# Performance work log

Measured on AMD Instinct MI355X. Metric: run time of the kernel, lower is better.

## Reference

```python
import jax, jax.numpy as jnp
import numpy as np

# dims
T, N, F, B = 8, 100000, 128, 4096        # snapshots, graph nodes, in_features, seed batch
S1, S2 = 5, 2                             # sampling fanouts (sizes=[5,2])
H1, H2, O, C = 512, 64, 32, 2             # hids=[512,64], out_features, nchannels
TIME_MOD = 2
W_POS, W_NOPOS = 0.6, 0.4
V_TH = 1.0                                # invth=1


@jax.custom_vjp
def spike(v):
    # IF/LIF firing with threshold V_TH (spikingjelly-style heaviside)
    return (v >= V_TH).astype(v.dtype)

def _spike_fwd(v):
    return spike(v), v

def _spike_bwd(v, g):
    # triangle surrogate gradient, alpha=1.0
    return (g * jnp.maximum(0.0, 1.0 - jnp.abs(v - V_TH)),)

spike.defvjp(_spike_fwd, _spike_bwd)


def sinusoid_table(n_pos, d):
    # vectorized port of get_sinusoid_encoding_table
    pos = np.arange(n_pos, dtype=np.float32)[:, None]
    i = np.arange(d)[None, :]
    angle = pos / (10000.0 ** (2.0 * (i // 2) / d))
    tab = np.where(i % 2 == 0, np.sin(angle), np.cos(angle)).astype(np.float32)
    return jnp.asarray(tab)


def srga_single(h0, h1, h2, Ws1, Wn1, Ws2, Wn2):
    """2-layer sampled-SAGE with spiking activations (one snapshot).
    h0:[B,F] seeds, h1:[B*S1,F] hop1, h2:[B*S1*S2,F] hop2."""
    n0, n1 = h0.shape[0], h1.shape[0]
    # layer 1 applied at levels 0 and 1 (mean neighbor aggregation, no bias)
    agg0 = h1.reshape(n0, S1, -1).mean(axis=1)
    s0 = spike(h0 @ Ws1 + agg0 @ Wn1)            # [B, H1]
    agg1 = h2.reshape(n1, S2, -1).mean(axis=1)
    s1 = spike(h1 @ Ws1 + agg1 @ Wn1)            # [B*S1, H1]
    # layer 2 fuses level-1 spikes into seeds
    agg = s1.reshape(n0, S1, -1).mean(axis=1)
    return spike(s0 @ Ws2 + agg @ Wn2)            # [B, H2]


def temporal_attn(seq, w, b, pos):
    # seq: [T', B, H2]; matches TemporalAttention (softmax over time)
    if pos is not None:
        seq = seq + pos[:seq.shape[0], None, :]
    scores = jnp.einsum('tbh,ho->tbo', seq, w) + b       # [T',B,1]
    wts = jax.nn.softmax(scores, axis=0)[..., 0]          # [T',B]
    return jnp.einsum('tbh,tb->bh', seq, wts)             # [B,H2]


def setup_inputs():
    key = jax.random.key(0)
    ks = jax.random.split(key, 14)
    nodes = jax.random.randint(ks[0], (B,), 0, N)
    hop1_idx = jax.random.randint(ks[1], (T, B * S1), 0, N)
    hop2_idx = jax.random.randint(ks[2], (T, B * S1 * S2), 0, N)
    x = jax.random.normal(ks[3], (T, N, F), dtype=jnp.float32)
    inp = {
        'nodes': nodes, 'hop1_idx': hop1_idx, 'hop2_idx': hop2_idx, 'x': x,
        'Wself1': jax.random.normal(ks[4], (C, F, H1), jnp.float32) / np.sqrt(F).astype(np.float32),
        'Wnbr1': jax.random.normal(ks[5], (C, F, H1), jnp.float32) / np.sqrt(F).astype(np.float32),
        'Wself2': jax.random.normal(ks[6], (C, H1, H2), jnp.float32) / np.sqrt(H1).astype(np.float32),
        'Wnbr2': jax.random.normal(ks[7], (C, H1, H2), jnp.float32) / np.sqrt(H1).astype(np.float32),
        'attn_pos_w': jax.random.normal(ks[8], (C, H2, 1), jnp.float32) / np.sqrt(H2).astype(np.float32),
        'attn_pos_b': jax.random.normal(ks[9], (C, 1), jnp.float32) * 0.01,
        'attn_nopos_w': jax.random.normal(ks[10], (C, H2, 1), jnp.float32) / np.sqrt(H2).astype(np.float32),
        'attn_nopos_b': jax.random.normal(ks[11], (C, 1), jnp.float32) * 0.01,
        'mtg_w': jax.random.normal(ks[12], (H2, O), jnp.float32) / np.sqrt(H2).astype(np.float32),
        'mtg_b': jax.random.normal(ks[13], (O,), jnp.float32) * 0.01,
    }
    return inp


def reference(nodes, hop1_idx, hop2_idx, x, Wself1, Wnbr1, Wself2, Wnbr2,
              attn_pos_w, attn_pos_b, attn_nopos_w, attn_nopos_b, mtg_w, mtg_b):
    tidx = jnp.arange(T)
    # irregular gathers per snapshot (the memory-bound hot path)
    h0 = x[tidx[:, None], nodes[None, :]]     # [T, B, F]
    h1 = x[tidx[:, None], hop1_idx]           # [T, B*S1, F]
    h2 = x[tidx[:, None], hop2_idx]           # [T, B*S1*S2, F]
    pos_tab = sinusoid_table(T, H2)
    channel_embs = []
    for c in range(C):
        if c == 0:
            hs = (h0, h1, h2)                 # channel 0: every step
        else:
            hs = (h0[::TIME_MOD], h1[::TIME_MOD], h2[::TIME_MOD])  # channel 1: t % time_mod == 0
        outs = jax.vmap(
            lambda a, b_, d_, c=c: srga_single(a, b_, d_, Wself1[c], Wnbr1[c], Wself2[c], Wnbr2[c])
        )(*hs)                                # [T', B, H2]
        emb_pos = temporal_attn(outs, attn_pos_w[c], attn_pos_b[c], pos_tab)
        emb_nopos = temporal_attn(outs, attn_nopos_w[c], attn_nopos_b[c], None)
        channel_embs.append(W_POS * emb_pos + W_NOPOS * emb_nopos)
    stacked = jnp.stack(channel_embs, axis=0).mean(axis=0)  # [B, H2]
    return stacked @ mtg_w + mtg_b                          # [B, O]
```

## Files before the change

### kernel.cpp

```cpp
#include <hip/hip_runtime.h>
#include <math.h>

typedef _Float16 f16;
typedef _Float16 f16x8 __attribute__((ext_vector_type(8)));
typedef float f32x4 __attribute__((ext_vector_type(4)));

#define T_ 8
#define NNODES 100000
#define F_ 128
#define B_ 4096
#define S1_ 5
#define S2_ 2
#define H1_ 512
#define H2_ 64
#define O_ 32
#define M1 (B_ + B_*S1_)
#define K1 (2*F_)
#define NZ 12

__device__ __forceinline__ float wsum64(float v) {
#pragma unroll
  for (int o = 32; o > 0; o >>= 1) v += __shfl_xor(v, o, 64);
  return v;
}

__global__ __launch_bounds__(512) void postab_kernel(float* __restrict__ postab) {
  int i = threadIdx.x;
  int p = i >> 6, d = i & 63;
  double ang = (double)p / pow(10000.0, (2.0 * (double)(d >> 1)) / 64.0);
  postab[i] = (float)((d & 1) ? cos(ang) : sin(ang));
}

__global__ __launch_bounds__(256)
void prep_w(const float* __restrict__ Ws1, const float* __restrict__ Wn1,
            f16* __restrict__ Bth, f16* __restrict__ Btl) {
  const int bid = blockIdx.x;
  const int c = bid >> 9, n = bid & 511;
  const int k = threadIdx.x;
  float wv = (k < F_) ? Ws1[((size_t)c * F_ + k) * H1_ + n]
                      : Wn1[((size_t)c * F_ + (k - F_)) * H1_ + n];
  f16 hi = (f16)wv;
  f16 lo = (f16)((wv - (float)hi) * 2048.0f);
  size_t o = ((size_t)c * H1_ + n) * K1 + k;
  Bth[o] = hi; Btl[o] = lo;
}

__global__ __launch_bounds__(256)
void prep_w2(const float* __restrict__ Ws2, const float* __restrict__ Wn2,
             f16* __restrict__ B2h, f16* __restrict__ B2l) {
  const int c = blockIdx.x >> 6, n = blockIdx.x & 63;
#pragma unroll
  for (int q = 0; q < 4; ++q) {
    const int k = q * 256 + threadIdx.x;
    float v = (k < H1_) ? Ws2[((size_t)c * H1_ + k) * H2_ + n]
                        : 0.2f * Wn2[((size_t)c * H1_ + (k - H1_)) * H2_ + n];
    f16 hi = (f16)v;
    f16 lo = (f16)((v - (float)hi) * 2048.0f);
    size_t o = ((size_t)c * H2_ + n) * 1024 + k;
    B2h[o] = hi; B2l[o] = lo;
  }
}

__global__ __launch_bounds__(256) void gather_kernel(
    const int* __restrict__ nodes, const int* __restrict__ hop1,
    const int* __restrict__ hop2, const float* __restrict__ x,
    f16* __restrict__ Ah, f16* __restrict__ Al)
{
  const int t = blockIdx.y;
  const int r = blockIdx.x * 4 + (threadIdx.x >> 6);
  const int lane = threadIdx.x & 63;
  const int fo = (lane & 31) << 2;
  const bool hpart = lane < 32;
  const float* xt = x + (size_t)t * NNODES * F_;
  float4 v;
  if (r < B_) {
    if (hpart) {
      v = *(const float4*)(xt + (size_t)nodes[r] * F_ + fo);
    } else {
      v = make_float4(0.f, 0.f, 0.f, 0.f);
#pragma unroll
      for (int s = 0; s < S1_; ++s) {
        int idx = hop1[t * (B_ * S1_) + r * S1_ + s];
        float4 u = *(const float4*)(xt + (size_t)idx * F_ + fo);
        v.x += u.x; v.y += u.y; v.z += u.z; v.w += u.w;
      }
      v.x /= 5.0f; v.y /= 5.0f; v.z /= 5.0f; v.w /= 5.0f;
    }
  } else {
    const int j = r - B_;
    if (hpart) {
      v = *(const float4*)(xt + (size_t)hop1[t * (B_ * S1_) + j] * F_ + fo);
    } else {
      v = make_float4(0.f, 0.f, 0.f, 0.f);
#pragma unroll
      for (int s = 0; s < S2_; ++s) {
        int idx = hop2[t * (B_ * S1_ * S2_) + j * S2_ + s];
        float4 u = *(const float4*)(xt + (size_t)idx * F_ + fo);
        v.x += u.x; v.y += u.y; v.z += u.z; v.w += u.w;
      }
      v.x *= 0.5f; v.y *= 0.5f; v.z *= 0.5f; v.w *= 0.5f;
    }
  }
  union { f16 h[4]; uint2 u; } H, L;
  float vv[4] = {v.x, v.y, v.z, v.w};
#pragma unroll
  for (int e = 0; e < 4; ++e) {
    f16 hi = (f16)vv[e];
    H.h[e] = hi;
    L.h[e] = (f16)((vv[e] - (float)hi) * 2048.0f);
  }
  const size_t base = ((size_t)t * M1 + r) * K1 + 4 * lane;
  *(uint2*)(Ah + base) = H.u;
  *(uint2*)(Al + base) = L.u;
}

__global__ __launch_bounds__(512)
void gemm1_mfma(const f16* __restrict__ Ah, const f16* __restrict__ Al,
                const f16* __restrict__ Bth, const f16* __restrict__ Btl,
                unsigned char* __restrict__ Sbase)
{
  const int hid = blockIdx.x + 4 * blockIdx.y + 384 * blockIdx.z;
  const int xcd = hid & 7, ii = hid >> 3;
  const int nblk = ii & 3;
  const int pair = xcd * 144 + (ii >> 2);
  const int yblk = pair % 96;
  const int z    = pair / 96;

  const int t = (z < 8) ? z : 2 * (z - 8);
  const int c = (z < 8) ? 0 : 1;
  const int m0 = yblk * 256;
  const int n0 = nblk * 128;
  const int tid = threadIdx.x;
  const int lane = tid & 63;
  const int w = tid >> 6;
  const int wr = w >> 1, wc = w & 1;

  __shared__ f16 lds[3][24576];

  const f16* tbAh = Ah  + (size_t)t * M1 * K1;
  const f16* tbAl = Al  + (size_t)t * M1 * K1;
  const f16* tbBh = Bth + (size_t)c * H1_ * K1;
  const f16* tbBl = Btl + (size_t)c * H1_ * K1;

  const f16* srcp[6];
#pragma unroll
  for (int q = 0; q < 6; ++q) {
    const int u = q * 512 + tid;
    const f16* base; int row, grow;
    if (u < 1024)      { base = tbAh; row = u >> 2;          grow = m0 + row; }
    else if (u < 2048) { base = tbAl; row = (u - 1024) >> 2; grow = m0 + row; }
    else if (u < 2560) { base = tbBh; row = (u - 2048) >> 2; grow = n0 + row; }
    else               { base = tbBl; row = (u - 2560) >> 2; grow = n0 + row; }
    const int kc = (u & 3) ^ ((row >> 1) & 3);
    srcp[q] = base + (size_t)grow * K1 + kc * 8;
  }

  auto stage = [&](int buf) {
#pragma unroll
    for (int q = 0; q < 6; ++q) {
      __builtin_amdgcn_global_load_lds(
          (const __attribute__((address_space(1))) void*)srcp[q],
          (__attribute__((address_space(3))) void*)((char*)lds + buf * 49152 + (q * 8 + w) * 1024),
          16, 0, 0);
      srcp[q] += 32;
    }
  };

  f32x4 accm[4][4], accc[4][4];
#pragma unroll
  for (int i = 0; i < 4; ++i)
#pragma unroll
    for (int j = 0; j < 4; ++j) {
      accm[i][j] = (f32x4){0.f, 0.f, 0.f, 0.f};
      accc[i][j] = (f32x4){0.f, 0.f, 0.f, 0.f};
    }

  const int kg = lane >> 4;
  const int lr = lane & 15;
  const int ks = (kg ^ ((lr >> 1) & 3)) * 8;

  stage(0);
  stage(1);
  asm volatile("s_waitcnt vmcnt(6)" ::: "memory");
  __builtin_amdgcn_s_barrier();
  __builtin_amdgcn_sched_barrier(0);

#pragma unroll
  for (int kt = 0; kt < 8; ++kt) {
    const int cur = kt % 3;
    const f16* bufp = &lds[cur][0];

    f16x8 ah[4], bh[4], al[4];
#pragma unroll
    for (int i = 0; i < 4; ++i) ah[i] = *(const f16x8*)(bufp + (wr * 64 + i * 16 + lr) * 32 + ks);
#pragma unroll
    for (int j = 0; j < 4; ++j) bh[j] = *(const f16x8*)(bufp + 16384 + (wc * 64 + j * 16 + lr) * 32 + ks);
#pragma unroll
    for (int i = 0; i < 4; ++i) al[i] = *(const f16x8*)(bufp + 8192 + (wr * 64 + i * 16 + lr) * 32 + ks);
    if (kt < 6) stage((kt + 2) % 3);

    __builtin_amdgcn_s_setprio(1);
#pragma unroll
    for (int j = 0; j < 4; ++j)
#pragma unroll
      for (int i = 0; i < 4; ++i)
        accm[i][j] = __builtin_amdgcn_mfma_f32_16x16x32_f16(ah[i], bh[j], accm[i][j], 0, 0, 0);
    __builtin_amdgcn_s_setprio(0);

    __builtin_amdgcn_s_setprio(1);
#pragma unroll
    for (int j = 0; j < 4; ++j)
#pragma unroll
      for (int i = 0; i < 4; ++i)
        accc[i][j] = __builtin_amdgcn_mfma_f32_16x16x32_f16(al[i], bh[j], accc[i][j], 0, 0, 0);
    __builtin_amdgcn_s_setprio(0);

    f16x8 bl[4];
#pragma unroll
    for (int j = 0; j < 4; ++j) bl[j] = *(const f16x8*)(bufp + 20480 + (wc * 64 + j * 16 + lr) * 32 + ks);
    __builtin_amdgcn_s_setprio(1);
#pragma unroll
    for (int j = 0; j < 4; ++j)
#pragma unroll
      for (int i = 0; i < 4; ++i)
        accc[i][j] = __builtin_amdgcn_mfma_f32_16x16x32_f16(ah[i], bl[j], accc[i][j], 0, 0, 0);
    __builtin_amdgcn_s_setprio(0);

    if (kt < 6) {
      asm volatile("s_waitcnt vmcnt(6)" ::: "memory");
      __builtin_amdgcn_s_barrier();
      __builtin_amdgcn_sched_barrier(0);
    } else if (kt == 6) {
      asm volatile("s_waitcnt vmcnt(0)" ::: "memory");
      __builtin_amdgcn_s_barrier();
      __builtin_amdgcn_sched_barrier(0);
    }
  }

  unsigned char* S = Sbase + (size_t)z * M1 * H1_;
#pragma unroll
  for (int i = 0; i < 4; ++i)
#pragma unroll
    for (int j = 0; j < 4; ++j) {
      const int n = n0 + wc * 64 + j * 16 + lr;
#pragma unroll
      for (int r = 0; r < 4; ++r) {
        const int m = m0 + wr * 64 + i * 16 + kg * 4 + r;
        float v = accm[i][j][r] + accc[i][j][r] * 4.8828125e-4f;
        S[(size_t)m * H1_ + n] = (v >= 1.0f) ? 1 : 0;
      }
    }
}

__global__ __launch_bounds__(256)
void gemm2_fused(const unsigned char* __restrict__ Sbase,
                 const f16* __restrict__ B2h, const f16* __restrict__ B2l,
                 unsigned char* __restrict__ outsbase)
{
  const int z = blockIdx.y;
  const int c = (z < 8) ? 0 : 1;
  const int m0 = blockIdx.x * 128;
  const int tid = threadIdx.x;
  const int lane = tid & 63;
  const int wv = tid >> 6;

  __shared__ f16 lds2[2][8192];

  const unsigned char* Sz = Sbase + (size_t)z * M1 * H1_;
  const f16* Bhc = B2h + (size_t)c * H2_ * 1024;
  const f16* Blc = B2l + (size_t)c * H2_ * 1024;

  const f16* srcB[2];
#pragma unroll
  for (int q = 0; q < 2; ++q) {
    const int v = q * 256 + tid;
    if (v < 256) {
      const int k8 = v >> 6, row = v & 63;
      srcB[q] = Bhc + (size_t)row * 1024 + k8 * 8;
    } else {
      const int v2 = v - 256, k8 = v2 >> 6, row = v2 & 63;
      srcB[q] = Blc + (size_t)row * 1024 + k8 * 8;
    }
  }
  auto stageB = [&](int buf) {
#pragma unroll
    for (int q = 0; q < 2; ++q) {
      __builtin_amdgcn_global_load_lds(
          (const __attribute__((address_space(1))) void*)srcB[q],
          (__attribute__((address_space(3))) void*)((char*)lds2 + buf * 16384 + 8192 + q * 4096 + wv * 1024),
          16, 0, 0);
      srcB[q] += 32;
    }
  };

  const int arow = tid >> 1;
  const int ahalf = tid & 1;
  const int k8b = ahalf * 2;

  auto loadS = [&](int kt, uint4* regs) {
    if (kt < 16) {
      regs[0] = *(const uint4*)(Sz + (size_t)(m0 + arow) * H1_ + kt * 32 + ahalf * 16);
    } else {
      const int k0 = (kt - 16) * 32 + ahalf * 16;
#pragma unroll
      for (int s = 0; s < S1_; ++s)
        regs[s] = *(const uint4*)(Sz + ((size_t)B_ + (size_t)(m0 + arow) * S1_ + s) * H1_ + k0);
    }
  };
  auto writeA = [&](int buf, int kt, const uint4* regs) {
    uint4 b;
    if (kt < 16) {
      b = regs[0];
    } else {
      b.x = regs[0].x + regs[1].x + regs[2].x + regs[3].x + regs[4].x;
      b.y = regs[0].y + regs[1].y + regs[2].y + regs[3].y + regs[4].y;
      b.z = regs[0].z + regs[1].z + regs[2].z + regs[3].z + regs[4].z;
      b.w = regs[0].w + regs[1].w + regs[2].w + regs[3].w + regs[4].w;
    }
    union { uint4 v; unsigned char by[16]; } U; U.v = b;
    union { f16 h[8]; uint4 v; } P0, P1;
#pragma unroll
    for (int e = 0; e < 8; ++e) {
      P0.h[e] = (f16)(int)U.by[e];
      P1.h[e] = (f16)(int)U.by[8 + e];
    }
    f16* dst = &lds2[buf][0];
    *(uint4*)(dst + ((size_t)k8b * 128 + arow) * 8)       = P0.v;
    *(uint4*)(dst + ((size_t)(k8b + 1) * 128 + arow) * 8) = P1.v;
  };

  f32x4 acch[2][4], accl[2][4];
#pragma unroll
  for (int i = 0; i < 2; ++i)
#pragma unroll
    for (int j = 0; j < 4; ++j) {
      acch[i][j] = (f32x4){0.f, 0.f, 0.f, 0.f};
      accl[i][j] = (f32x4){0.f, 0.f, 0.f, 0.f};
    }

  const int kg = lane >> 4;
  const int lr = lane & 15;

  {
    uint4 regs[5];
    loadS(0, regs);
    stageB(0);
    writeA(0, 0, regs);
  }
  __syncthreads();

#pragma unroll 1
  for (int kt = 0; kt < 32; ++kt) {
    const int cur = kt & 1;
    uint4 regs[5];
    if (kt < 31) {
      stageB(cur ^ 1);
      loadS(kt + 1, regs);
    }

    f16x8 a[2];
#pragma unroll
    for (int i = 0; i < 2; ++i)
      a[i] = *(const f16x8*)&lds2[cur][(size_t)(kg * 128 + wv * 32 + i * 16 + lr) * 8];
#pragma unroll
    for (int j = 0; j < 4; ++j) {
      f16x8 bh = *(const f16x8*)&lds2[cur][4096 + (size_t)(kg * 64 + j * 16 + lr) * 8];
      f16x8 bl = *(const f16x8*)&lds2[cur][6144 + (size_t)(kg * 64 + j * 16 + lr) * 8];
#pragma unroll
      for (int i = 0; i < 2; ++i) {
        acch[i][j] = __builtin_amdgcn_mfma_f32_16x16x32_f16(a[i], bh, acch[i][j], 0, 0, 0);
        accl[i][j] = __builtin_amdgcn_mfma_f32_16x16x32_f16(a[i], bl, accl[i][j], 0, 0, 0);
      }
    }
    if (kt < 31) writeA(cur ^ 1, kt + 1, regs);
    __syncthreads();
  }

  unsigned char* outs = outsbase + (size_t)z * B_ * H2_;
#pragma unroll
  for (int i = 0; i < 2; ++i)
#pragma unroll
    for (int j = 0; j < 4; ++j) {
      const int n = j * 16 + lr;
#pragma unroll
      for (int r = 0; r < 4; ++r) {
        const int m = m0 + wv * 32 + i * 16 + kg * 4 + r;
        float v = acch[i][j][r] + accl[i][j][r] * 4.8828125e-4f;
        outs[(size_t)m * H2_ + n] = (v >= 1.0f) ? 1 : 0;
      }
    }
}

__global__ __launch_bounds__(256)
void final_kernel(const unsigned char* __restrict__ outsbase,
                  const float* __restrict__ postab,
                  const float* __restrict__ apw, const float* __restrict__ apb,
                  const float* __restrict__ anw, const float* __restrict__ anb,
                  const float* __restrict__ mtgw, const float* __restrict__ mtgb,
                  float* __restrict__ out)
{
  const int b = blockIdx.x * 4 + (threadIdx.x >> 6);
  const int lane = threadIdx.x & 63;
  float stacked = 0.f;
#pragma unroll
  for (int c = 0; c < 2; ++c) {
    const int Tc = c ? 4 : 8;
    const int zb = c ? 8 : 0;
    const float wp = apw[c * H2_ + lane];
    const float wn = anw[c * H2_ + lane];
    float seqv[8], sp[8], sn[8];
#pragma unroll
    for (int tt = 0; tt < Tc; ++tt) {
      const float sv = (float)outsbase[((size_t)(zb + tt) * B_ + b) * H2_ + lane];
      seqv[tt] = sv;
      sp[tt] = wsum64((sv + postab[tt * H2_ + lane]) * wp);
      sn[tt] = wsum64(sv * wn);
    }
    const float bp = apb[c], bn = anb[c];
    float mp = -3.4e38f, mn = -3.4e38f;
#pragma unroll
    for (int tt = 0; tt < Tc; ++tt) {
      sp[tt] += bp; sn[tt] += bn;
      mp = fmaxf(mp, sp[tt]); mn = fmaxf(mn, sn[tt]);
    }
    float ep[8], en[8], sump = 0.f, sumn = 0.f;
#pragma unroll
    for (int tt = 0; tt < Tc; ++tt) {
      ep[tt] = expf(sp[tt] - mp);
      en[tt] = expf(sn[tt] - mn);
      sump += ep[tt]; sumn += en[tt];
    }
    float embp = 0.f, embn = 0.f;
#pragma unroll
    for (int tt = 0; tt < Tc; ++tt) {
      embp += (seqv[tt] + postab[tt * H2_ + lane]) * (ep[tt] / sump);
      embn += seqv[tt] * (en[tt] / sumn);
    }
    stacked += 0.5f * (0.6f * embp + 0.4f * embn);
  }
  float res = 0.f;
#pragma unroll
  for (int o = 0; o < O_; ++o) {
    float r = wsum64(stacked * mtgw[lane * O_ + o]);
    if (lane == o) res = r;
  }
  if (lane < O_) out[(size_t)b * O_ + lane] = res + mtgb[lane];
}

extern "C" void kernel_launch(void* const* d_in, const int* in_sizes, int n_in,
                              void* d_out, int out_size, void* d_ws, size_t ws_size,
                              hipStream_t stream)
{
  const int*   nodes  = (const int*)d_in[0];
  const int*   hop1   = (const int*)d_in[1];
  const int*   hop2   = (const int*)d_in[2];
  const float* x      = (const float*)d_in[3];
  const float* Wself1 = (const float*)d_in[4];
  const float* Wnbr1  = (const float*)d_in[5];
  const float* Wself2 = (const float*)d_in[6];
  const float* Wnbr2  = (const float*)d_in[7];
  const float* apw    = (const float*)d_in[8];
  const float* apb    = (const float*)d_in[9];
  const float* anw    = (const float*)d_in[10];
  const float* anb    = (const float*)d_in[11];
  const float* mtgw   = (const float*)d_in[12];
  const float* mtgb   = (const float*)d_in[13];
  float* out = (float*)d_out;

  char* ws = (char*)d_ws;
  size_t off = 0;
  float* postab = (float*)(ws + off);               off += 4096;
  f16* Ahb = (f16*)(ws + off);                      off += (size_t)T_ * M1 * K1 * 2;
  f16* Alb = (f16*)(ws + off);                      off += (size_t)T_ * M1 * K1 * 2;
  unsigned char* Sbase = (unsigned char*)(ws + off); off += (size_t)NZ * M1 * H1_;
  unsigned char* outsb = (unsigned char*)(ws + off); off += (size_t)NZ * B_ * H2_;
  if (ws_size < off) return;

  f16* Bth = (f16*)outsb;
  f16* Btl = Bth + (size_t)2 * H1_ * K1;
  f16* B2h = Alb;
  f16* B2l = B2h + (size_t)2 * H2_ * 1024;

  hipLaunchKernelGGL(postab_kernel, dim3(1), dim3(512), 0, stream, postab);
  hipLaunchKernelGGL(prep_w, dim3(1024), dim3(256), 0, stream, Wself1, Wnbr1, Bth, Btl);
  hipLaunchKernelGGL(gather_kernel, dim3(M1 / 4, T_), dim3(256), 0, stream,
                     nodes, hop1, hop2, x, Ahb, Alb);
  hipLaunchKernelGGL(gemm1_mfma, dim3(4, 96, NZ), dim3(512), 0, stream,
                     Ahb, Alb, Bth, Btl, Sbase);
  hipLaunchKernelGGL(prep_w2, dim3(128), dim3(256), 0, stream, Wself2, Wnbr2, B2h, B2l);
  hipLaunchKernelGGL(gemm2_fused, dim3(B_ / 128, NZ), dim3(256), 0, stream,
                     Sbase, B2h, B2l, outsb);
  hipLaunchKernelGGL(final_kernel, dim3(B_ / 4), dim3(256), 0, stream,
                     outsb, postab, apw, apb, anw, anb, mtgw, mtgb, out);
}
```

Before: 461.3 us.

## Interleave LDS reads, global prefetch and MFMA in four phases per k-tile

Splits each k-tile of the fp16 hi/lo split GEMM into four phases, one per B column block. Each phase loads its bh/bl fragments, issues a third of the next stage's global-to-LDS loads, then runs 12 MFMAs, with barriers around each phase in a ping-pong style schedule. The goal is finer interleaving of memory and matrix work so MFMA issue is not stalled behind bulk LDS reads. It adds two barriers per phase (8 per k-tile instead of 1), which may add synchronization overhead.

```diff
diff --git a/kernel.cpp b/kernel.cpp
--- a/kernel.cpp
+++ b/kernel.cpp
@@ -155,9 +155,9 @@
     srcp[q] = base + (size_t)grow * K1 + kc * 8;
   }
 
-  auto stage = [&](int buf) {
-#pragma unroll
-    for (int q = 0; q < 6; ++q) {
+  auto stage2 = [&](int buf, int pr) {
+#pragma unroll
+    for (int q = pr * 2; q < pr * 2 + 2; ++q) {
       __builtin_amdgcn_global_load_lds(
           (const __attribute__((address_space(1))) void*)srcp[q],
           (__attribute__((address_space(3))) void*)((char*)lds + buf * 49152 + (q * 8 + w) * 1024),
@@ -179,8 +179,8 @@
   const int lr = lane & 15;
   const int ks = (kg ^ ((lr >> 1) & 3)) * 8;
 
-  stage(0);
-  stage(1);
+  stage2(0, 0); stage2(0, 1); stage2(0, 2);
+  stage2(1, 0); stage2(1, 1); stage2(1, 2);
   asm volatile("s_waitcnt vmcnt(6)" ::: "memory");
   __builtin_amdgcn_s_barrier();
   __builtin_amdgcn_sched_barrier(0);
@@ -188,50 +188,45 @@
 #pragma unroll
   for (int kt = 0; kt < 8; ++kt) {
     const int cur = kt % 3;
+    const int nxt = (kt + 2) % 3;
     const f16* bufp = &lds[cur][0];
 
-    f16x8 ah[4], bh[4], al[4];
-#pragma unroll
-    for (int i = 0; i < 4; ++i) ah[i] = *(const f16x8*)(bufp + (wr * 64 + i * 16 + lr) * 32 + ks);
-#pragma unroll
-    for (int j = 0; j < 4; ++j) bh[j] = *(const f16x8*)(bufp + 16384 + (wc * 64 + j * 16 + lr) * 32 + ks);
-#pragma unroll
-    for (int i = 0; i < 4; ++i) al[i] = *(const f16x8*)(bufp + 8192 + (wr * 64 + i * 16 + lr) * 32 + ks);
-    if (kt < 6) stage((kt + 2) % 3);
-
-    __builtin_amdgcn_s_setprio(1);
-#pragma unroll
-    for (int j = 0; j < 4; ++j)
+    f16x8 ah[4], al[4];
+#pragma unroll
+    for (int p = 0; p < 4; ++p) {
+      if (p == 0) {
+#pragma unroll
+        for (int i = 0; i < 4; ++i) ah[i] = *(const f16x8*)(bufp + (wr * 64 + i * 16 + lr) * 32 + ks);
+#pragma unroll
+        for (int i = 0; i < 4; ++i) al[i] = *(const f16x8*)(bufp + 8192 + (wr * 64 + i * 16 + lr) * 32 + ks);
+      }
+      f16x8 bh = *(const f16x8*)(bufp + 16384 + (wc * 64 + p * 16 + lr) * 32 + ks);
+      f16x8 bl = *(const f16x8*)(bufp + 20480 + (wc * 64 + p * 16 + lr) * 32 + ks);
+      if (kt < 6 && p < 3) stage2(nxt, p);
+
+      __builtin_amdgcn_s_barrier();
+      asm volatile("s_waitcnt lgkmcnt(0)" ::: "memory");
+      __builtin_amdgcn_sched_barrier(0);
+
+      __builtin_amdgcn_s_setprio(1);
 #pragma unroll
       for (int i = 0; i < 4; ++i)
-        accm[i][j] = __builtin_amdgcn_mfma_f32_16x16x32_f16(ah[i], bh[j], accm[i][j], 0, 0, 0);
-    __builtin_amdgcn_s_setprio(0);
-
-    __builtin_amdgcn_s_setprio(1);
-#pragma unroll
-    for (int j = 0; j < 4; ++j)
+        accm[i][p] = __builtin_amdgcn_mfma_f32_16x16x32_f16(ah[i], bh, accm[i][p], 0, 0, 0);
 #pragma unroll
       for (int i = 0; i < 4; ++i)
-        accc[i][j] = __builtin_amdgcn_mfma_f32_16x16x32_f16(al[i], bh[j], accc[i][j], 0, 0, 0);
-    __builtin_amdgcn_s_setprio(0);
-
-    f16x8 bl[4];
-#pragma unroll
-    for (int j = 0; j < 4; ++j) bl[j] = *(const f16x8*)(bufp + 20480 + (wc * 64 + j * 16 + lr) * 32 + ks);
-    __builtin_amdgcn_s_setprio(1);
-#pragma unroll
-    for (int j = 0; j < 4; ++j)
+        accc[i][p] = __builtin_amdgcn_mfma_f32_16x16x32_f16(al[i], bh, accc[i][p], 0, 0, 0);
 #pragma unroll
       for (int i = 0; i < 4; ++i)
-        accc[i][j] = __builtin_amdgcn_mfma_f32_16x16x32_f16(ah[i], bl[j], accc[i][j], 0, 0, 0);
-    __builtin_amdgcn_s_setprio(0);
-
-    if (kt < 6) {
-      asm volatile("s_waitcnt vmcnt(6)" ::: "memory");
-      __builtin_amdgcn_s_barrier();
-      __builtin_amdgcn_sched_barrier(0);
-    } else if (kt == 6) {
-      asm volatile("s_waitcnt vmcnt(0)" ::: "memory");
+        accc[i][p] = __builtin_amdgcn_mfma_f32_16x16x32_f16(ah[i], bl, accc[i][p], 0, 0, 0);
+      __builtin_amdgcn_s_setprio(0);
+
+      if (p == 3) {
+        if (kt < 6) {
+          asm volatile("s_waitcnt vmcnt(6)" ::: "memory");
+        } else if (kt == 6) {
+          asm volatile("s_waitcnt vmcnt(0)" ::: "memory");
+        }
+      }
       __builtin_amdgcn_s_barrier();
       __builtin_amdgcn_sched_barrier(0);
     }
```

Result: no change. 460.2 us (-0.2%).
